# Kernel optimization log

Hardware: AMD Instinct MI355X
Metric: run time of the kernel (lower is better)

## Reference

```python
import jax, jax.numpy as jnp
import numpy as np

B, N, DIM, H = 8, 1024, 768, 12
DH = DIM // H          # 64
LATENT = 32
EPS = 1e-5


def setup_inputs() -> dict:
    key = jax.random.key(0)
    ks = jax.random.split(key, 6)
    s = 0.02
    return {
        "x": jax.random.normal(ks[0], (B, N, DIM), jnp.float32),
        "Wq": jax.random.normal(ks[1], (DIM, DIM), jnp.float32) * s,
        "Wkv": jax.random.normal(ks[2], (DIM, DIM), jnp.float32) * s,
        "Wo_ctx": jax.random.normal(ks[3], (DIM, DIM), jnp.float32) * s,
        "bo_ctx": jnp.zeros((DIM,), jnp.float32),
        "Wo_lat": jax.random.normal(ks[4], (DIM, DIM), jnp.float32) * s,
        "bo_lat": jnp.zeros((DIM,), jnp.float32),
        "ln_g": jnp.ones((DH,), jnp.float32),
        "ln_b": jnp.zeros((DH,), jnp.float32),
    }


def _heads(t):
    # 'b n (h d) -> (b h) n d'
    b, n, _ = t.shape
    return t.reshape(b, n, H, DH).transpose(0, 2, 1, 3).reshape(b * H, n, DH)


def _merge(t, b):
    # '(b h) n d -> b n (h d)'
    _, n, dh = t.shape
    return t.reshape(b, H, n, dh).transpose(0, 2, 1, 3).reshape(b, n, H * dh)


def _ln(v, g, bta):
    mu = v.mean(-1, keepdims=True)
    var = ((v - mu) ** 2).mean(-1, keepdims=True)
    return (v - mu) * jax.lax.rsqrt(var + EPS) * g + bta


def _rope(t):
    # rotary embedding over full head dim (lucidrains-style half rotation)
    n, dh = t.shape[-2], t.shape[-1]
    inv = 1.0 / (10000.0 ** (jnp.arange(0, dh, 2, dtype=jnp.float32) / dh))
    f = jnp.arange(n, dtype=jnp.float32)[:, None] * inv[None, :]   # [n, dh/2]
    f = jnp.concatenate([f, f], -1)[None]                          # [1, n, dh]
    x1, x2 = jnp.split(t, 2, -1)
    rot = jnp.concatenate([-x2, x1], -1)
    return t * jnp.cos(f) + rot * jnp.sin(f)


def reference(x, Wq, Wkv, Wo_ctx, bo_ctx, Wo_lat, bo_lat, ln_g, ln_b):
    b, n, _ = x.shape
    ctx = n - LATENT  # context_len
    q = _heads(x @ Wq)
    kv = _heads(x @ Wkv)
    # layer_num == 0: rotary applied to both q and kv
    q = _rope(q)
    kv = _rope(kv)
    q = q * (DH ** -0.5)
    q_lat, q_ctx = q[:, ctx:], q[:, :ctx]
    kv_ctx = kv[:, :ctx]
    lkv = _ln(kv, ln_g, ln_b)
    lkv_ctx = _ln(kv_ctx, ln_g, ln_b)
    # latent queries attend to ALL positions; context attends to context only
    attn_lat = jax.nn.softmax(jnp.einsum('bid,bkd->bik', q_lat, kv), axis=-1)
    attn_ctx = jax.nn.softmax(jnp.einsum('bid,bkd->bik', q_ctx, kv_ctx), axis=-1)
    out_lat = _merge(jnp.einsum('bik,bkd->bid', attn_lat, lkv), b) @ Wo_lat + bo_lat
    out_ctx = _merge(jnp.einsum('bik,bkd->bid', attn_ctx, lkv_ctx), b) @ Wo_ctx + bo_ctx
    return jnp.concatenate([out_ctx, out_lat], axis=1)  # [b, n, dim]
```

## Files before the change

kernel.cpp:

```cpp
#include <hip/hip_runtime.h>

#define B_    8
#define N_    1024
#define DIM_  768
#define H_    12
#define DH_   64
#define CTX_  992
#define BH_   (B_ * H_)
#define EPS_  1e-5f
#define WSZ_  (DIM_ * DIM_)
#define PS_   72

typedef unsigned short ush;
typedef __attribute__((ext_vector_type(8))) short bf8_t;
typedef __attribute__((ext_vector_type(4))) float f4_t;

__device__ __forceinline__ float b2f(ush u) {
    return __uint_as_float(((unsigned)u) << 16);
}
__device__ __forceinline__ ush f2b(float f) {
    unsigned u = __float_as_uint(f);
    u += 0x7fffu + ((u >> 16) & 1u);
    return (ush)(u >> 16);
}
__device__ __forceinline__ void gload_lds16(const void* g, void* l) {
    __builtin_amdgcn_global_load_lds(
        (const __attribute__((address_space(1))) void*)g,
        (__attribute__((address_space(3))) void*)l, 16, 0, 0);
}

__global__ __launch_bounds__(256) void cast_x(
    const float* __restrict__ X, ush* __restrict__ Xb)
{
    const int i4 = blockIdx.x * 256 + threadIdx.x;
    float4 v = *(const float4*)&X[(size_t)i4 * 4];
    ushort4 o;
    o.x = f2b(v.x); o.y = f2b(v.y); o.z = f2b(v.z); o.w = f2b(v.w);
    *(ushort4*)&Xb[(size_t)i4 * 4] = o;
}

__global__ __launch_bounds__(256) void cast_wt(
    const float* __restrict__ W0, const float* __restrict__ W1,
    const float* __restrict__ W2, const float* __restrict__ W3,
    ush* __restrict__ T0, ush* __restrict__ T1,
    ush* __restrict__ T2, ush* __restrict__ T3)
{
    const float* W = (blockIdx.z == 0) ? W0 : (blockIdx.z == 1) ? W1 :
                     (blockIdx.z == 2) ? W2 : W3;
    ush* Wt        = (blockIdx.z == 0) ? T0 : (blockIdx.z == 1) ? T1 :
                     (blockIdx.z == 2) ? T2 : T3;
    const int i0 = blockIdx.y * 64;
    const int j0 = blockIdx.x * 64;
    const int tid = threadIdx.x;

    __shared__ ush T[64][65];

    const int r4 = tid >> 4, c = (tid & 15) << 2;
    #pragma unroll
    for (int g = 0; g < 4; ++g) {
        const int r = r4 + g * 16;
        float4 v = *(const float4*)&W[(size_t)(i0 + r) * DIM_ + j0 + c];
        T[r][c + 0] = f2b(v.x); T[r][c + 1] = f2b(v.y);
        T[r][c + 2] = f2b(v.z); T[r][c + 3] = f2b(v.w);
    }
    __syncthreads();
    const int nl = tid >> 2, k0l = (tid & 3) << 4;
    #pragma unroll
    for (int g = 0; g < 4; ++g) {
        ushort4 o;
        o.x = T[k0l + 4 * g + 0][nl]; o.y = T[k0l + 4 * g + 1][nl];
        o.z = T[k0l + 4 * g + 2][nl]; o.w = T[k0l + 4 * g + 3][nl];
        *(ushort4*)&Wt[(size_t)(j0 + nl) * DIM_ + i0 + k0l + 4 * g] = o;
    }
}

__global__ __launch_bounds__(256, 3) void gemm_qkv_mfma(
    const ush* __restrict__ Xb, const ush* __restrict__ Wt0,
    const ush* __restrict__ Wt1, ush* __restrict__ Q16, ush* __restrict__ K16,
    ush* __restrict__ Vn, const float* __restrict__ ln_g,
    const float* __restrict__ ln_b)
{
    const int z   = blockIdx.z;
    const ush* Bt = z ? Wt1 : Wt0;
    const int m0 = blockIdx.y * 128, c0 = blockIdx.x * 128;
    const int tid = threadIdx.x;
    const int w = tid >> 6, lane = tid & 63, l15 = lane & 15, quad = lane >> 4;
    const int wm = w >> 1, wn = w & 1;

    __shared__ __align__(16) ush As[128 * 32];
    __shared__ __align__(16) ush Bs[128 * 32];

    const int slot0 = w * 2 * 64 + lane;
    const int srow0 = slot0 >> 2, scc0 = (slot0 & 3) ^ (srow0 & 3);
    const int slot1 = slot0 + 64;
    const int srow1 = slot1 >> 2, scc1 = (slot1 & 3) ^ (srow1 & 3);

    f4_t acc[4][4];
    #pragma unroll
    for (int i = 0; i < 4; ++i)
        #pragma unroll
        for (int j = 0; j < 4; ++j)
            #pragma unroll
            for (int r = 0; r < 4; ++r) acc[i][j][r] = 0.f;

    for (int k0 = 0; k0 < DIM_; k0 += 32) {
        __syncthreads();
        gload_lds16((const char*)Xb + (size_t)(m0 + srow0) * (DIM_ * 2) + k0 * 2 + scc0 * 16,
                    (char*)As + slot0 * 16);
        gload_lds16((const char*)Bt + (size_t)(c0 + srow0) * (DIM_ * 2) + k0 * 2 + scc0 * 16,
                    (char*)Bs + slot0 * 16);
        gload_lds16((const char*)Xb + (size_t)(m0 + srow1) * (DIM_ * 2) + k0 * 2 + scc1 * 16,
                    (char*)As + slot1 * 16);
        gload_lds16((const char*)Bt + (size_t)(c0 + srow1) * (DIM_ * 2) + k0 * 2 + scc1 * 16,
                    (char*)Bs + slot1 * 16);
        __syncthreads();

        const int sq = (quad ^ (l15 & 3)) * 8;
        bf8_t af[4];
        #pragma unroll
        for (int mi = 0; mi < 4; ++mi)
            af[mi] = *(const bf8_t*)&As[(wm * 64 + mi * 16 + l15) * 32 + sq];
        #pragma unroll
        for (int ni = 0; ni < 4; ++ni) {
            bf8_t bfr = *(const bf8_t*)&Bs[(wn * 64 + ni * 16 + l15) * 32 + sq];
            #pragma unroll
            for (int mi = 0; mi < 4; ++mi)
                acc[mi][ni] = __builtin_amdgcn_mfma_f32_16x16x32_bf16(
                    af[mi], bfr, acc[mi][ni], 0, 0, 0);
        }
    }

    const float inv0 = __expf(-(float)l15 * (9.210340371976184f / 32.0f));
    const float inv1 = inv0 * 0.01f;
    const int h  = (c0 >> 6) + wn;
    const int b  = (m0 + wm * 64) >> 10;
    const int nb = (m0 + wm * 64) & 1023;

    #pragma unroll
    for (int mi = 0; mi < 4; ++mi) {
        #pragma unroll
        for (int r = 0; r < 4; ++r) {
            const int n = nb + mi * 16 + quad * 4 + r;
            float sn0, cs0, sn1, cs1;
            __sincosf((float)n * inv0, &sn0, &cs0);
            __sincosf((float)n * inv1, &sn1, &cs1);
            {
                float a = acc[mi][0][r], p = acc[mi][2][r];
                acc[mi][0][r] = a * cs0 - p * sn0;
                acc[mi][2][r] = p * cs0 + a * sn0;
            }
            {
                float a = acc[mi][1][r], p = acc[mi][3][r];
                acc[mi][1][r] = a * cs1 - p * sn1;
                acc[mi][3][r] = p * cs1 + a * sn1;
            }
        }
    }

    if (z == 0) {
        #pragma unroll
        for (int mi = 0; mi < 4; ++mi)
            #pragma unroll
            for (int ni = 0; ni < 4; ++ni)
                #pragma unroll
                for (int r = 0; r < 4; ++r) {
                    const int n = nb + mi * 16 + quad * 4 + r;
                    const int d = ni * 16 + l15;
                    Q16[(((size_t)b * H_ + h) * N_ + n) * DH_ + d] =
                        f2b(acc[mi][ni][r] * 0.125f);
                }
    } else {
        float g4[4], b4[4];
        #pragma unroll
        for (int ni = 0; ni < 4; ++ni) {
            g4[ni] = ln_g[ni * 16 + l15];
            b4[ni] = ln_b[ni * 16 + l15];
        }
        #pragma unroll
        for (int mi = 0; mi < 4; ++mi)
            #pragma unroll
            for (int r = 0; r < 4; ++r) {
                const int n = nb + mi * 16 + quad * 4 + r;
                const size_t rowoff = (((size_t)b * H_ + h) * N_ + n) * DH_;
                float s = (acc[mi][0][r] + acc[mi][1][r]) +
                          (acc[mi][2][r] + acc[mi][3][r]);
                #pragma unroll
                for (int o = 8; o >= 1; o >>= 1) s += __shfl_xor(s, o);
                const float mu = s * (1.0f / 64.0f);
                float sq = 0.f;
                #pragma unroll
                for (int ni = 0; ni < 4; ++ni) {
                    const float dv = acc[mi][ni][r] - mu;
                    sq = fmaf(dv, dv, sq);
                }
                #pragma unroll
                for (int o = 8; o >= 1; o >>= 1) sq += __shfl_xor(sq, o);
                const float rstd = rsqrtf(sq * (1.0f / 64.0f) + EPS_);
                #pragma unroll
                for (int ni = 0; ni < 4; ++ni) {
                    const int d = ni * 16 + l15;
                    K16[rowoff + d] = f2b(acc[mi][ni][r]);
                    Vn[rowoff + d]  = f2b((acc[mi][ni][r] - mu) * rstd * g4[ni] + b4[ni]);
                }
            }
    }
}

__global__ __launch_bounds__(256) void transpose_v(
    const ush* __restrict__ Vn, ush* __restrict__ Vt)
{
    const int bh = blockIdx.y;
    const int n0 = blockIdx.x * 64;
    const int tid = threadIdx.x;

    __shared__ ush T[64][65];

    const int r4 = tid >> 4, c = (tid & 15) << 2;
    #pragma unroll
    for (int g = 0; g < 4; ++g) {
        const int r = r4 + g * 16;
        ushort4 v = *(const ushort4*)&Vn[((size_t)bh * N_ + n0 + r) * DH_ + c];
        T[r][c + 0] = v.x; T[r][c + 1] = v.y; T[r][c + 2] = v.z; T[r][c + 3] = v.w;
    }
    __syncthreads();
    const int dl = tid >> 2, G0 = (tid & 3) << 2;
    #pragma unroll
    for (int g = 0; g < 4; ++g) {
        const int G = G0 + g;
        ushort4 o;
        o.x = T[G][dl]; o.y = T[16 + G][dl];
        o.z = T[32 + G][dl]; o.w = T[48 + G][dl];
        *(ushort4*)&Vt[((size_t)bh * DH_ + dl) * N_ + n0 + 4 * G] = o;
    }
}

__global__ __launch_bounds__(256, 4) void attn_mfma(
    const ush* __restrict__ Qh, const ush* __restrict__ Kh,
    const ush* __restrict__ Vt, ush* __restrict__ ATT)
{
    const int bh = blockIdx.y;
    const int q0 = blockIdx.x * 128;
    const int tid = threadIdx.x;
    const int w = tid >> 6, lane = tid & 63, l15 = lane & 15, quad = lane >> 4;

    __shared__ __align__(16) ush Ks[64 * 64];
    __shared__ __align__(16) ush Vs[64 * 64];
    __shared__ __align__(16) ush QPs[128 * PS_];

    const int sw8 = (l15 & 7);

    {
        const char* qg = (const char*)(Qh + ((size_t)bh * N_ + q0) * DH_);
        #pragma unroll
        for (int i = 0; i < 4; ++i) {
            const int slot = (w * 4 + i) * 64 + lane;
            const int row = slot >> 3, cc = (slot & 7) ^ (row & 7);
            gload_lds16(qg + (size_t)row * 128 + cc * 16, (char*)QPs + slot * 16);
        }
    }
    __syncthreads();

    bf8_t aq[2][2];
    #pragma unroll
    for (int mi = 0; mi < 2; ++mi)
        #pragma unroll
        for (int ks = 0; ks < 2; ++ks)
            aq[mi][ks] = *(const bf8_t*)&QPs[(w * 32 + mi * 16 + l15) * 64 +
                                             (((ks * 4 + quad) ^ sw8) * 8)];

    f4_t O[2][4];
    float l_[2][4];
    #pragma unroll
    for (int mi = 0; mi < 2; ++mi)
        #pragma unroll
        for (int r = 0; r < 4; ++r) {
            l_[mi][r] = 0.f;
            #pragma unroll
            for (int ni = 0; ni < 4; ++ni) O[mi][ni][r] = 0.f;
        }

    const char* kg = (const char*)(Kh + (size_t)bh * N_ * DH_);
    const char* vg = (const char*)(Vt + (size_t)bh * DH_ * N_);

    for (int t = 0; t < 16; ++t) {
        __syncthreads();
        #pragma unroll
        for (int i = 0; i < 2; ++i) {
            const int slot = (w * 2 + i) * 64 + lane;
            const int row = slot >> 3, cc = (slot & 7) ^ (row & 7);
            gload_lds16(kg + (size_t)(t * 64 + row) * 128 + cc * 16,
                        (char*)Ks + slot * 16);
            gload_lds16(vg + (size_t)row * (N_ * 2) + t * 128 + cc * 16,
                        (char*)Vs + slot * 16);
        }
        __syncthreads();

        f4_t s[2][4];
        #pragma unroll
        for (int mi = 0; mi < 2; ++mi)
            #pragma unroll
            for (int ni = 0; ni < 4; ++ni)
                #pragma unroll
                for (int r = 0; r < 4; ++r) s[mi][ni][r] = 0.f;
        #pragma unroll
        for (int ks = 0; ks < 2; ++ks)
            #pragma unroll
            for (int ni = 0; ni < 4; ++ni) {
                bf8_t bk = *(const bf8_t*)&Ks[(ni * 16 + l15) * 64 +
                                              (((ks * 4 + quad) ^ sw8) * 8)];
                #pragma unroll
                for (int mi = 0; mi < 2; ++mi)
                    s[mi][ni] = __builtin_amdgcn_mfma_f32_16x16x32_bf16(
                        aq[mi][ks], bk, s[mi][ni], 0, 0, 0);
            }

        if (t == 15) {
            #pragma unroll
            for (int mi = 0; mi < 2; ++mi)
                #pragma unroll
                for (int r = 0; r < 4; ++r) {
                    const int row = q0 + w * 32 + mi * 16 + quad * 4 + r;
                    if (row < CTX_) { s[mi][2][r] = -1e30f; s[mi][3][r] = -1e30f; }
                }
        }

        #pragma unroll
        for (int mi = 0; mi < 2; ++mi)
            #pragma unroll
            for (int r = 0; r < 4; ++r) {
                float p0 = __expf(s[mi][0][r]), p1 = __expf(s[mi][1][r]);
                float p2 = __expf(s[mi][2][r]), p3 = __expf(s[mi][3][r]);
                l_[mi][r] += (p0 + p1) + (p2 + p3);
                ushort4 pk;
                pk.x = f2b(p0); pk.y = f2b(p1); pk.z = f2b(p2); pk.w = f2b(p3);
                *(ushort4*)&QPs[(w * 32 + mi * 16 + quad * 4 + r) * PS_ + l15 * 4] = pk;
            }

        #pragma unroll
        for (int ks = 0; ks < 2; ++ks) {
            bf8_t ap[2];
            #pragma unroll
            for (int mi = 0; mi < 2; ++mi)
                ap[mi] = *(const bf8_t*)&QPs[(w * 32 + mi * 16 + l15) * PS_ +
                                             ks * 32 + quad * 8];
            #pragma unroll
            for (int ni = 0; ni < 4; ++ni) {
                bf8_t bv = *(const bf8_t*)&Vs[(ni * 16 + l15) * 64 +
                                              (((ks * 4 + quad) ^ sw8) * 8)];
                #pragma unroll
                for (int mi = 0; mi < 2; ++mi)
                    O[mi][ni] = __builtin_amdgcn_mfma_f32_16x16x32_bf16(
                        ap[mi], bv, O[mi][ni], 0, 0, 0);
            }
        }
    }

    const int b = bh / H_, h = bh % H_;
    #pragma unroll
    for (int mi = 0; mi < 2; ++mi)
        #pragma unroll
        for (int r = 0; r < 4; ++r) {
            float l = l_[mi][r];
            #pragma unroll
            for (int o = 8; o >= 1; o >>= 1) l += __shfl_xor(l, o);
            const float inv = 1.0f / l;
            const int row = q0 + w * 32 + mi * 16 + quad * 4 + r;
            #pragma unroll
            for (int ni = 0; ni < 4; ++ni)
                ATT[((size_t)b * N_ + row) * DIM_ + h * DH_ + ni * 16 + l15] =
                    f2b(O[mi][ni][r] * inv);
        }
}

__global__ __launch_bounds__(256, 2) void gemm_o_mfma(
    const ush* __restrict__ ATT, const ush* __restrict__ Btc,
    const float* __restrict__ biasc, const ush* __restrict__ Btl,
    const float* __restrict__ biasl, float* __restrict__ out)
{
    const int lat = (blockIdx.y >= 64);
    const ush* Bt    = lat ? Btl : Btc;
    const float* bias = lat ? biasl : biasc;
    const int m0 = (lat ? (blockIdx.y - 64) : blockIdx.y) * 128;
    const int c0 = blockIdx.x * 128;
    const int tid = threadIdx.x;
    const int w = tid >> 6, lane = tid & 63, l15 = lane & 15, quad = lane >> 4;
    const int wm = w >> 1, wn = w & 1;

    __shared__ __align__(16) ush As[128 * 32];
    __shared__ __align__(16) ush Bs[128 * 32];

    const int slot0 = w * 2 * 64 + lane;
    const int srow0 = slot0 >> 2, scc0 = (slot0 & 3) ^ (srow0 & 3);
    const int slot1 = slot0 + 64;
    const int srow1 = slot1 >> 2, scc1 = (slot1 & 3) ^ (srow1 & 3);
    const int am0 = m0 + srow0, am1 = m0 + srow1;
    const int grow0 = lat ? (((am0 >> 5) << 10) + CTX_ + (am0 & 31)) : am0;
    const int grow1 = lat ? (((am1 >> 5) << 10) + CTX_ + (am1 & 31)) : am1;

    f4_t acc[4][4];
    #pragma unroll
    for (int i = 0; i < 4; ++i)
        #pragma unroll
        for (int j = 0; j < 4; ++j)
            #pragma unroll
            for (int r = 0; r < 4; ++r) acc[i][j][r] = 0.f;

    for (int k0 = 0; k0 < DIM_; k0 += 32) {
        __syncthreads();
        gload_lds16((const char*)ATT + (size_t)grow0 * (DIM_ * 2) + k0 * 2 + scc0 * 16,
                    (char*)As + slot0 * 16);
        gload_lds16((const char*)Bt + (size_t)(c0 + srow0) * (DIM_ * 2) + k0 * 2 + scc0 * 16,
                    (char*)Bs + slot0 * 16);
        gload_lds16((const char*)ATT + (size_t)grow1 * (DIM_ * 2) + k0 * 2 + scc1 * 16,
                    (char*)As + slot1 * 16);
        gload_lds16((const char*)Bt + (size_t)(c0 + srow1) * (DIM_ * 2) + k0 * 2 + scc1 * 16,
                    (char*)Bs + slot1 * 16);
        __syncthreads();

        const int sq = (quad ^ (l15 & 3)) * 8;
        bf8_t af[4];
        #pragma unroll
        for (int mi = 0; mi < 4; ++mi)
            af[mi] = *(const bf8_t*)&As[(wm * 64 + mi * 16 + l15) * 32 + sq];
        #pragma unroll
        for (int ni = 0; ni < 4; ++ni) {
            bf8_t bfr = *(const bf8_t*)&Bs[(wn * 64 + ni * 16 + l15) * 32 + sq];
            #pragma unroll
            for (int mi = 0; mi < 4; ++mi)
                acc[mi][ni] = __builtin_amdgcn_mfma_f32_16x16x32_bf16(
                    af[mi], bfr, acc[mi][ni], 0, 0, 0);
        }
    }

    #pragma unroll
    for (int mi = 0; mi < 4; ++mi)
        #pragma unroll
        for (int ni = 0; ni < 4; ++ni) {
            const int c = c0 + wn * 64 + ni * 16 + l15;
            const float bs = bias[c];
            #pragma unroll
            for (int r = 0; r < 4; ++r) {
                const int m = m0 + wm * 64 + mi * 16 + quad * 4 + r;
                if (!lat && (m & 1023) >= CTX_) continue;
                const int grow = lat ? (((m >> 5) << 10) + CTX_ + (m & 31)) : m;
                out[(size_t)grow * DIM_ + c] = acc[mi][ni][r] + bs;
            }
        }
}

extern "C" void kernel_launch(void* const* d_in, const int* in_sizes, int n_in,
                              void* d_out, int out_size, void* d_ws, size_t ws_size,
                              hipStream_t stream) {
    const float* X      = (const float*)d_in[0];
    const float* Wq     = (const float*)d_in[1];
    const float* Wkv    = (const float*)d_in[2];
    const float* Wo_ctx = (const float*)d_in[3];
    const float* bo_ctx = (const float*)d_in[4];
    const float* Wo_lat = (const float*)d_in[5];
    const float* bo_lat = (const float*)d_in[6];
    const float* ln_g   = (const float*)d_in[7];
    const float* ln_b   = (const float*)d_in[8];
    float* out = (float*)d_out;

    ush* ws = (ush*)d_ws;
    const size_t E = (size_t)BH_ * N_ * DH_;
    ush* Xb  = ws;
    ush* Q16 = ws + E;
    ush* K16 = ws + 2 * E;
    ush* Vn  = ws + 3 * E;
    ush* Vt  = ws + 4 * E;
    ush* Wt0 = ws + 5 * E;
    ush* Wt1 = Wt0 + WSZ_;
    ush* Wt2 = Wt1 + WSZ_;
    ush* Wt3 = Wt2 + WSZ_;
    ush* ATT = Xb;

    cast_x<<<dim3((int)(E / 1024)), 256, 0, stream>>>(X, Xb);
    cast_wt<<<dim3(12, 12, 4), 256, 0, stream>>>(Wq, Wkv, Wo_ctx, Wo_lat,
                                                 Wt0, Wt1, Wt2, Wt3);
    gemm_qkv_mfma<<<dim3(6, 64, 2), 256, 0, stream>>>(Xb, Wt0, Wt1, Q16, K16,
                                                      Vn, ln_g, ln_b);
    transpose_v<<<dim3(16, BH_), 256, 0, stream>>>(Vn, Vt);
    attn_mfma<<<dim3(8, BH_), 256, 0, stream>>>(Q16, K16, Vt, ATT);
    gemm_o_mfma<<<dim3(6, 66), 256, 0, stream>>>(ATT, Wt2, bo_ctx, Wt3, bo_lat, out);
}
```

Measured before the change: 200.2 us.

## Split attention keys across warps, halve output GEMM tile, fuse cast kernels

Merges the x cast and the weight-transpose cast into a single launch to drop one kernel launch. In the attention kernel, each pair of warps now shares 64 query rows, and each warp handles half of every 64-key tile. The two partial outputs and row sums are combined through shared memory at the end. This raises per-warp MFMA reuse of the key fragments but adds a reduction step and lowers occupancy to 3 blocks. The output GEMM uses 64-row tiles with twice as many blocks for better CU coverage. The V transpose also changes its column interleave order.

New measurement: 232.1 us. 1.16x slower.

```diff
diff --git a/kernel.cpp b/kernel.cpp
--- a/kernel.cpp
+++ b/kernel.cpp
@@ -9,7 +9,7 @@
 #define BH_   (B_ * H_)
 #define EPS_  1e-5f
 #define WSZ_  (DIM_ * DIM_)
-#define PS_   72
+#define PSW_  40
 
 typedef unsigned short ush;
 typedef __attribute__((ext_vector_type(8))) short bf8_t;
@@ -29,31 +29,31 @@
         (__attribute__((address_space(3))) void*)l, 16, 0, 0);
 }
 
-__global__ __launch_bounds__(256) void cast_x(
-    const float* __restrict__ X, ush* __restrict__ Xb)
-{
-    const int i4 = blockIdx.x * 256 + threadIdx.x;
-    float4 v = *(const float4*)&X[(size_t)i4 * 4];
-    ushort4 o;
-    o.x = f2b(v.x); o.y = f2b(v.y); o.z = f2b(v.z); o.w = f2b(v.w);
-    *(ushort4*)&Xb[(size_t)i4 * 4] = o;
-}
-
-__global__ __launch_bounds__(256) void cast_wt(
+__global__ __launch_bounds__(256) void cast_all(
+    const float* __restrict__ X, ush* __restrict__ Xb,
     const float* __restrict__ W0, const float* __restrict__ W1,
     const float* __restrict__ W2, const float* __restrict__ W3,
     ush* __restrict__ T0, ush* __restrict__ T1,
     ush* __restrict__ T2, ush* __restrict__ T3)
 {
-    const float* W = (blockIdx.z == 0) ? W0 : (blockIdx.z == 1) ? W1 :
-                     (blockIdx.z == 2) ? W2 : W3;
-    ush* Wt        = (blockIdx.z == 0) ? T0 : (blockIdx.z == 1) ? T1 :
-                     (blockIdx.z == 2) ? T2 : T3;
-    const int i0 = blockIdx.y * 64;
-    const int j0 = blockIdx.x * 64;
+    __shared__ ush T[64][65];
+    const int bid = blockIdx.x;
     const int tid = threadIdx.x;
 
-    __shared__ ush T[64][65];
+    if (bid < 6144) {
+        const int i4 = bid * 256 + tid;
+        float4 v = *(const float4*)&X[(size_t)i4 * 4];
+        ushort4 o;
+        o.x = f2b(v.x); o.y = f2b(v.y); o.z = f2b(v.z); o.w = f2b(v.w);
+        *(ushort4*)&Xb[(size_t)i4 * 4] = o;
+        return;
+    }
+    const int t = bid - 6144;
+    const int z = t / 144, rem = t % 144;
+    const int i0 = (rem / 12) * 64;
+    const int j0 = (rem % 12) * 64;
+    const float* W = (z == 0) ? W0 : (z == 1) ? W1 : (z == 2) ? W2 : W3;
+    ush* Wt        = (z == 0) ? T0 : (z == 1) ? T1 : (z == 2) ? T2 : T3;
 
     const int r4 = tid >> 4, c = (tid & 15) << 2;
     #pragma unroll
@@ -227,14 +227,15 @@
     #pragma unroll
     for (int g = 0; g < 4; ++g) {
         const int G = G0 + g;
+        const int base = ((G >> 3) << 5) + ((G & 7) << 1);
         ushort4 o;
-        o.x = T[G][dl]; o.y = T[16 + G][dl];
-        o.z = T[32 + G][dl]; o.w = T[48 + G][dl];
+        o.x = T[base][dl];      o.y = T[base + 16][dl];
+        o.z = T[base + 1][dl];  o.w = T[base + 17][dl];
         *(ushort4*)&Vt[((size_t)bh * DH_ + dl) * N_ + n0 + 4 * G] = o;
     }
 }
 
-__global__ __launch_bounds__(256, 4) void attn_mfma(
+__global__ __launch_bounds__(256, 3) void attn_mfma(
     const ush* __restrict__ Qh, const ush* __restrict__ Kh,
     const ush* __restrict__ Vt, ush* __restrict__ ATT)
 {
@@ -242,12 +243,16 @@
     const int q0 = blockIdx.x * 128;
     const int tid = threadIdx.x;
     const int w = tid >> 6, lane = tid & 63, l15 = lane & 15, quad = lane >> 4;
-
-    __shared__ __align__(16) ush Ks[64 * 64];
-    __shared__ __align__(16) ush Vs[64 * 64];
-    __shared__ __align__(16) ush QPs[128 * PS_];
-
-    const int sw8 = (l15 & 7);
+    const int wq = w >> 1, wk = w & 1;
+
+    __shared__ __align__(16) ush SMEM[18432];
+    ush* Ks = SMEM;
+    ush* Vs = SMEM + 4096;
+    ush* QP = SMEM + 8192;
+    float* LF = (float*)SMEM;
+    float* LL = (float*)SMEM + 8192;
+
+    const int sw8 = l15 & 7;
 
     {
         const char* qg = (const char*)(Qh + ((size_t)bh * N_ + q0) * DH_);
@@ -255,23 +260,24 @@
         for (int i = 0; i < 4; ++i) {
             const int slot = (w * 4 + i) * 64 + lane;
             const int row = slot >> 3, cc = (slot & 7) ^ (row & 7);
-            gload_lds16(qg + (size_t)row * 128 + cc * 16, (char*)QPs + slot * 16);
+            gload_lds16(qg + (size_t)row * 128 + cc * 16, (char*)QP + slot * 16);
         }
     }
     __syncthreads();
 
-    bf8_t aq[2][2];
-    #pragma unroll
-    for (int mi = 0; mi < 2; ++mi)
-        #pragma unroll
-        for (int ks = 0; ks < 2; ++ks)
-            aq[mi][ks] = *(const bf8_t*)&QPs[(w * 32 + mi * 16 + l15) * 64 +
-                                             (((ks * 4 + quad) ^ sw8) * 8)];
-
-    f4_t O[2][4];
-    float l_[2][4];
-    #pragma unroll
-    for (int mi = 0; mi < 2; ++mi)
+    bf8_t aq[4][2];
+    #pragma unroll
+    for (int mi = 0; mi < 4; ++mi)
+        #pragma unroll
+        for (int ks = 0; ks < 2; ++ks) {
+            const int row = wq * 64 + mi * 16 + l15;
+            aq[mi][ks] = *(const bf8_t*)&QP[row * 64 + (((ks * 4 + quad) ^ sw8) * 8)];
+        }
+
+    f4_t O[4][4];
+    float l_[4][4];
+    #pragma unroll
+    for (int mi = 0; mi < 4; ++mi)
         #pragma unroll
         for (int r = 0; r < 4; ++r) {
             l_[mi][r] = 0.f;
@@ -281,6 +287,7 @@
 
     const char* kg = (const char*)(Kh + (size_t)bh * N_ * DH_);
     const char* vg = (const char*)(Vt + (size_t)bh * DH_ * N_);
+    ush* Pw = QP + w * 2560;
 
     for (int t = 0; t < 16; ++t) {
         __syncthreads();
@@ -295,111 +302,137 @@
         }
         __syncthreads();
 
-        f4_t s[2][4];
-        #pragma unroll
-        for (int mi = 0; mi < 2; ++mi)
-            #pragma unroll
-            for (int ni = 0; ni < 4; ++ni)
+        f4_t s[4][2];
+        #pragma unroll
+        for (int mi = 0; mi < 4; ++mi)
+            #pragma unroll
+            for (int ni = 0; ni < 2; ++ni)
                 #pragma unroll
                 for (int r = 0; r < 4; ++r) s[mi][ni][r] = 0.f;
         #pragma unroll
         for (int ks = 0; ks < 2; ++ks)
             #pragma unroll
-            for (int ni = 0; ni < 4; ++ni) {
-                bf8_t bk = *(const bf8_t*)&Ks[(ni * 16 + l15) * 64 +
+            for (int ni = 0; ni < 2; ++ni) {
+                bf8_t bk = *(const bf8_t*)&Ks[(wk * 32 + ni * 16 + l15) * 64 +
                                               (((ks * 4 + quad) ^ sw8) * 8)];
                 #pragma unroll
-                for (int mi = 0; mi < 2; ++mi)
+                for (int mi = 0; mi < 4; ++mi)
                     s[mi][ni] = __builtin_amdgcn_mfma_f32_16x16x32_bf16(
                         aq[mi][ks], bk, s[mi][ni], 0, 0, 0);
             }
 
-        if (t == 15) {
-            #pragma unroll
-            for (int mi = 0; mi < 2; ++mi)
+        if (t == 15 && wk == 1) {
+            #pragma unroll
+            for (int mi = 0; mi < 4; ++mi)
                 #pragma unroll
                 for (int r = 0; r < 4; ++r) {
-                    const int row = q0 + w * 32 + mi * 16 + quad * 4 + r;
-                    if (row < CTX_) { s[mi][2][r] = -1e30f; s[mi][3][r] = -1e30f; }
+                    const int row = q0 + wq * 64 + mi * 16 + quad * 4 + r;
+                    if (row < CTX_) { s[mi][0][r] = -1e30f; s[mi][1][r] = -1e30f; }
                 }
         }
 
         #pragma unroll
-        for (int mi = 0; mi < 2; ++mi)
+        for (int mi = 0; mi < 4; ++mi)
             #pragma unroll
             for (int r = 0; r < 4; ++r) {
                 float p0 = __expf(s[mi][0][r]), p1 = __expf(s[mi][1][r]);
-                float p2 = __expf(s[mi][2][r]), p3 = __expf(s[mi][3][r]);
-                l_[mi][r] += (p0 + p1) + (p2 + p3);
-                ushort4 pk;
-                pk.x = f2b(p0); pk.y = f2b(p1); pk.z = f2b(p2); pk.w = f2b(p3);
-                *(ushort4*)&QPs[(w * 32 + mi * 16 + quad * 4 + r) * PS_ + l15 * 4] = pk;
-            }
-
-        #pragma unroll
-        for (int ks = 0; ks < 2; ++ks) {
-            bf8_t ap[2];
-            #pragma unroll
-            for (int mi = 0; mi < 2; ++mi)
-                ap[mi] = *(const bf8_t*)&QPs[(w * 32 + mi * 16 + l15) * PS_ +
-                                             ks * 32 + quad * 8];
+                l_[mi][r] += p0 + p1;
+                ushort2 pk;
+                pk.x = f2b(p0); pk.y = f2b(p1);
+                *(ushort2*)&Pw[(mi * 16 + quad * 4 + r) * PSW_ + l15 * 2] = pk;
+            }
+
+        {
+            bf8_t ap[4];
+            #pragma unroll
+            for (int mi = 0; mi < 4; ++mi)
+                ap[mi] = *(const bf8_t*)&Pw[(mi * 16 + l15) * PSW_ + quad * 8];
             #pragma unroll
             for (int ni = 0; ni < 4; ++ni) {
                 bf8_t bv = *(const bf8_t*)&Vs[(ni * 16 + l15) * 64 +
-                                              (((ks * 4 + quad) ^ sw8) * 8)];
-                #pragma unroll
-                for (int mi = 0; mi < 2; ++mi)
+                                              (((wk * 4 + quad) ^ sw8) * 8)];
+                #pragma unroll
+                for (int mi = 0; mi < 4; ++mi)
                     O[mi][ni] = __builtin_amdgcn_mfma_f32_16x16x32_bf16(
                         ap[mi], bv, O[mi][ni], 0, 0, 0);
             }
         }
     }
 
-    const int b = bh / H_, h = bh % H_;
-    #pragma unroll
-    for (int mi = 0; mi < 2; ++mi)
+    #pragma unroll
+    for (int mi = 0; mi < 4; ++mi)
         #pragma unroll
         for (int r = 0; r < 4; ++r) {
             float l = l_[mi][r];
             #pragma unroll
             for (int o = 8; o >= 1; o >>= 1) l += __shfl_xor(l, o);
-            const float inv = 1.0f / l;
-            const int row = q0 + w * 32 + mi * 16 + quad * 4 + r;
-            #pragma unroll
-            for (int ni = 0; ni < 4; ++ni)
-                ATT[((size_t)b * N_ + row) * DIM_ + h * DH_ + ni * 16 + l15] =
-                    f2b(O[mi][ni][r] * inv);
-        }
-}
-
-__global__ __launch_bounds__(256, 2) void gemm_o_mfma(
+            l_[mi][r] = l;
+        }
+
+    __syncthreads();
+    if (wk) {
+        #pragma unroll
+        for (int mi = 0; mi < 4; ++mi)
+            #pragma unroll
+            for (int r = 0; r < 4; ++r) {
+                const int rl = mi * 16 + quad * 4 + r;
+                #pragma unroll
+                for (int ni = 0; ni < 4; ++ni)
+                    LF[wq * 4096 + rl * 64 + ni * 16 + l15] = O[mi][ni][r];
+                if (l15 == 0) LL[wq * 64 + rl] = l_[mi][r];
+            }
+    }
+    __syncthreads();
+    if (!wk) {
+        const int b = bh / H_, h = bh % H_;
+        #pragma unroll
+        for (int mi = 0; mi < 4; ++mi)
+            #pragma unroll
+            for (int r = 0; r < 4; ++r) {
+                const int rl = mi * 16 + quad * 4 + r;
+                const float inv = 1.0f / (l_[mi][r] + LL[wq * 64 + rl]);
+                const int row = q0 + wq * 64 + rl;
+                #pragma unroll
+                for (int ni = 0; ni < 4; ++ni) {
+                    const float v = (O[mi][ni][r] +
+                                     LF[wq * 4096 + rl * 64 + ni * 16 + l15]) * inv;
+                    ATT[((size_t)b * N_ + row) * DIM_ + h * DH_ + ni * 16 + l15] = f2b(v);
+                }
+            }
+    }
+}
+
+__global__ __launch_bounds__(256, 4) void gemm_o_mfma(
     const ush* __restrict__ ATT, const ush* __restrict__ Btc,
     const float* __restrict__ biasc, const ush* __restrict__ Btl,
     const float* __restrict__ biasl, float* __restrict__ out)
 {
-    const int lat = (blockIdx.y >= 64);
-    const ush* Bt    = lat ? Btl : Btc;
+    const int y = blockIdx.y;
+    const int lat = (y >= 128);
+    const ush* Bt     = lat ? Btl : Btc;
     const float* bias = lat ? biasl : biasc;
-    const int m0 = (lat ? (blockIdx.y - 64) : blockIdx.y) * 128;
     const int c0 = blockIdx.x * 128;
     const int tid = threadIdx.x;
     const int w = tid >> 6, lane = tid & 63, l15 = lane & 15, quad = lane >> 4;
     const int wm = w >> 1, wn = w & 1;
 
-    __shared__ __align__(16) ush As[128 * 32];
+    __shared__ __align__(16) ush As[64 * 32];
     __shared__ __align__(16) ush Bs[128 * 32];
 
-    const int slot0 = w * 2 * 64 + lane;
-    const int srow0 = slot0 >> 2, scc0 = (slot0 & 3) ^ (srow0 & 3);
-    const int slot1 = slot0 + 64;
-    const int srow1 = slot1 >> 2, scc1 = (slot1 & 3) ^ (srow1 & 3);
-    const int am0 = m0 + srow0, am1 = m0 + srow1;
-    const int grow0 = lat ? (((am0 >> 5) << 10) + CTX_ + (am0 & 31)) : am0;
-    const int grow1 = lat ? (((am1 >> 5) << 10) + CTX_ + (am1 & 31)) : am1;
-
-    f4_t acc[4][4];
-    #pragma unroll
-    for (int i = 0; i < 4; ++i)
+    const int arow = tid >> 2, acc0 = (tid & 3) ^ (arow & 3);
+    int agrow;
+    if (lat) {
+        const int lr = (y - 128) * 64 + arow;
+        agrow = ((lr >> 5) << 10) + CTX_ + (lr & 31);
+    } else {
+        agrow = y * 64 + arow;
+    }
+    const int bs0 = tid,        brow0 = bs0 >> 2, bcc0 = (bs0 & 3) ^ (brow0 & 3);
+    const int bs1 = tid + 256,  brow1 = bs1 >> 2, bcc1 = (bs1 & 3) ^ (brow1 & 3);
+
+    f4_t acc[2][4];
+    #pragma unroll
+    for (int i = 0; i < 2; ++i)
         #pragma unroll
         for (int j = 0; j < 4; ++j)
             #pragma unroll
@@ -407,42 +440,47 @@
 
     for (int k0 = 0; k0 < DIM_; k0 += 32) {
         __syncthreads();
-        gload_lds16((const char*)ATT + (size_t)grow0 * (DIM_ * 2) + k0 * 2 + scc0 * 16,
-                    (char*)As + slot0 * 16);
-        gload_lds16((const char*)Bt + (size_t)(c0 + srow0) * (DIM_ * 2) + k0 * 2 + scc0 * 16,
-                    (char*)Bs + slot0 * 16);
-        gload_lds16((const char*)ATT + (size_t)grow1 * (DIM_ * 2) + k0 * 2 + scc1 * 16,
-                    (char*)As + slot1 * 16);
-        gload_lds16((const char*)Bt + (size_t)(c0 + srow1) * (DIM_ * 2) + k0 * 2 + scc1 * 16,
-                    (char*)Bs + slot1 * 16);
+        gload_lds16((const char*)ATT + (size_t)agrow * (DIM_ * 2) + k0 * 2 + acc0 * 16,
+                    (char*)As + tid * 16);
+        gload_lds16((const char*)Bt + (size_t)(c0 + brow0) * (DIM_ * 2) + k0 * 2 + bcc0 * 16,
+                    (char*)Bs + bs0 * 16);
+        gload_lds16((const char*)Bt + (size_t)(c0 + brow1) * (DIM_ * 2) + k0 * 2 + bcc1 * 16,
+                    (char*)Bs + bs1 * 16);
         __syncthreads();
 
         const int sq = (quad ^ (l15 & 3)) * 8;
-        bf8_t af[4];
-        #pragma unroll
-        for (int mi = 0; mi < 4; ++mi)
-            af[mi] = *(const bf8_t*)&As[(wm * 64 + mi * 16 + l15) * 32 + sq];
+        bf8_t af[2];
+        #pragma unroll
+        for (int mi = 0; mi < 2; ++mi)
+            af[mi] = *(const bf8_t*)&As[(wm * 32 + mi * 16 + l15) * 32 + sq];
         #pragma unroll
         for (int ni = 0; ni < 4; ++ni) {
             bf8_t bfr = *(const bf8_t*)&Bs[(wn * 64 + ni * 16 + l15) * 32 + sq];
             #pragma unroll
-            for (int mi = 0; mi < 4; ++mi)
+            for (int mi = 0; mi < 2; ++mi)
                 acc[mi][ni] = __builtin_amdgcn_mfma_f32_16x16x32_bf16(
                     af[mi], bfr, acc[mi][ni], 0, 0, 0);
         }
     }
 
     #pragma unroll
-    for (int mi = 0; mi < 4; ++mi)
+    for (int mi = 0; mi < 2; ++mi)
         #pragma unroll
         for (int ni = 0; ni < 4; ++ni) {
             const int c = c0 + wn * 64 + ni * 16 + l15;
             const float bs = bias[c];
             #pragma unroll
             for (int r = 0; r < 4; ++r) {
-                const int m = m0 + wm * 64 + mi * 16 + quad * 4 + r;
-                if (!lat && (m & 1023) >= CTX_) continue;
-                const int grow = lat ? (((m >> 5) << 10) + CTX_ + (m & 31)) : m;
+                const int ml = wm * 32 + mi * 16 + quad * 4 + r;
+                int grow;
+                if (lat) {
+                    const int lr = (y - 128) * 64 + ml;
+                    grow = ((lr >> 5) << 10) + CTX_ + (lr & 31);
+                } else {
+                    const int m = y * 64 + ml;
+                    if ((m & 1023) >= CTX_) continue;
+                    grow = m;
+                }
                 out[(size_t)grow * DIM_ + c] = acc[mi][ni][r] + bs;
             }
         }
@@ -475,12 +513,11 @@
     ush* Wt3 = Wt2 + WSZ_;
     ush* ATT = Xb;
 
-    cast_x<<<dim3((int)(E / 1024)), 256, 0, stream>>>(X, Xb);
-    cast_wt<<<dim3(12, 12, 4), 256, 0, stream>>>(Wq, Wkv, Wo_ctx, Wo_lat,
-                                                 Wt0, Wt1, Wt2, Wt3);
+    cast_all<<<dim3(6144 + 576), 256, 0, stream>>>(X, Xb, Wq, Wkv, Wo_ctx,
+                                                   Wo_lat, Wt0, Wt1, Wt2, Wt3);
     gemm_qkv_mfma<<<dim3(6, 64, 2), 256, 0, stream>>>(Xb, Wt0, Wt1, Q16, K16,
                                                       Vn, ln_g, ln_b);
     transpose_v<<<dim3(16, BH_), 256, 0, stream>>>(Vn, Vt);
     attn_mfma<<<dim3(8, BH_), 256, 0, stream>>>(Q16, K16, Vt, ATT);
-    gemm_o_mfma<<<dim3(6, 66), 256, 0, stream>>>(ATT, Wt2, bo_ctx, Wt3, bo_lat, out);
-}
+    gemm_o_mfma<<<dim3(6, 132), 256, 0, stream>>>(ATT, Wt2, bo_ctx, Wt3, bo_lat, out);
+}
```
